# Kernel optimization log

Measured on AMD Instinct MI355X. Metric: run time of the kernel, lower is better.

## Reference

```python
import jax, jax.numpy as jnp
import numpy as np

N = 30000       # mesh nodes
E = 150000      # mesh edges
L = 128         # latent_size
STEPS = 5       # message_passing_steps
TW = 5          # time_window
TD = 2          # target_dim
NODE_IN = TD + 1 + 9   # u + load + node_type one-hot = 12
EDGE_IN = 2 + 1 + TD   # rel_mesh + dist + grad_u = 5


def _mlp(x, W1, b1, W2, b2, g, be):
    # Linear -> ReLU -> Linear -> ReLU -> LayerNorm (matches MLP module)
    h = jax.nn.relu(x @ W1 + b1)
    h = jax.nn.relu(h @ W2 + b2)
    mu = jnp.mean(h, axis=-1, keepdims=True)
    var = jnp.mean(jnp.square(h - mu), axis=-1, keepdims=True)
    return g * (h - mu) / jnp.sqrt(var + 1e-5) + be


def setup_inputs() -> dict:
    key = jax.random.key(0)
    ks = iter(jax.random.split(key, 64))
    def nrm(shape, s=0.05):
        return jax.random.normal(next(ks), shape, dtype=jnp.float32) * s
    inp = {}
    inp['mesh_pos'] = jax.random.normal(next(ks), (1, N, 2), dtype=jnp.float32)
    inp['node_type'] = jax.random.normal(next(ks), (1, N, 9), dtype=jnp.float32)
    inp['u'] = jax.random.normal(next(ks), (1, N, TD), dtype=jnp.float32)
    inp['load'] = jax.random.normal(next(ks), (1, N, 1), dtype=jnp.float32)
    inp['senders'] = jax.random.randint(next(ks), (E,), 0, N, dtype=jnp.int32)
    inp['receivers'] = jax.random.randint(next(ks), (E,), 0, N, dtype=jnp.int32)
    # node encoder MLP(12 -> 128)
    inp['enc_node_W1'] = nrm((NODE_IN, L)); inp['enc_node_b1'] = nrm((L,), 0.01)
    inp['enc_node_W2'] = nrm((L, L));       inp['enc_node_b2'] = nrm((L,), 0.01)
    inp['enc_node_g'] = jnp.ones((L,), jnp.float32); inp['enc_node_be'] = jnp.zeros((L,), jnp.float32)
    # edge encoder MLP(5 -> 128)
    inp['enc_edge_W1'] = nrm((EDGE_IN, L)); inp['enc_edge_b1'] = nrm((L,), 0.01)
    inp['enc_edge_W2'] = nrm((L, L));       inp['enc_edge_b2'] = nrm((L,), 0.01)
    inp['enc_edge_g'] = jnp.ones((L,), jnp.float32); inp['enc_edge_be'] = jnp.zeros((L,), jnp.float32)
    # STEPS GraphNetBlocks, params stacked along leading axis for lax.scan
    inp['blk_edge_W1'] = nrm((STEPS, 3 * L, L)); inp['blk_edge_b1'] = nrm((STEPS, L), 0.01)
    inp['blk_edge_W2'] = nrm((STEPS, L, L));     inp['blk_edge_b2'] = nrm((STEPS, L), 0.01)
    inp['blk_edge_g'] = jnp.ones((STEPS, L), jnp.float32); inp['blk_edge_be'] = jnp.zeros((STEPS, L), jnp.float32)
    inp['blk_node_W1'] = nrm((STEPS, 2 * L, L)); inp['blk_node_b1'] = nrm((STEPS, L), 0.01)
    inp['blk_node_W2'] = nrm((STEPS, L, L));     inp['blk_node_b2'] = nrm((STEPS, L), 0.01)
    inp['blk_node_g'] = jnp.ones((STEPS, L), jnp.float32); inp['blk_node_be'] = jnp.zeros((STEPS, L), jnp.float32)
    # decoder: Conv1d(L,8,1) -> Swish -> Conv1d(8, TD*TW, 1); kernel-size-1 conv == per-node linear
    inp['dec_W1'] = nrm((L, 8)); inp['dec_b1'] = nrm((8,), 0.01)
    inp['dec_W2'] = nrm((8, TD * TW)); inp['dec_b2'] = nrm((TD * TW,), 0.01)
    return inp


def reference(mesh_pos, node_type, u, load, senders, receivers,
              enc_node_W1, enc_node_b1, enc_node_W2, enc_node_b2, enc_node_g, enc_node_be,
              enc_edge_W1, enc_edge_b1, enc_edge_W2, enc_edge_b2, enc_edge_g, enc_edge_be,
              blk_edge_W1, blk_edge_b1, blk_edge_W2, blk_edge_b2, blk_edge_g, blk_edge_be,
              blk_node_W1, blk_node_b1, blk_node_W2, blk_node_b2, blk_node_g, blk_node_be,
              dec_W1, dec_b1, dec_W2, dec_b2):
    # --- encode ---
    node_feats = jnp.concatenate([u, load, node_type], axis=-1)        # [1,N,12]
    nl = _mlp(node_feats, enc_node_W1, enc_node_b1, enc_node_W2, enc_node_b2, enc_node_g, enc_node_be)
    rel = mesh_pos[:, senders] - mesh_pos[:, receivers]                # [1,E,2]
    dist = jnp.linalg.norm(rel, axis=-1, keepdims=True)                # [1,E,1]
    grad_u = u[:, senders] - u[:, receivers]                           # [1,E,2]
    ef = jnp.concatenate([rel, dist, grad_u], axis=-1)                 # [1,E,5]
    el = _mlp(ef, enc_edge_W1, enc_edge_b1, enc_edge_W2, enc_edge_b2, enc_edge_g, enc_edge_be)
    n_nodes = nl.shape[1]

    # --- process: GraphNetBlocks with residual connections ---
    def block(carry, p):
        nl, el = carry
        edge_in = jnp.concatenate([nl[:, senders], nl[:, receivers], el], axis=-1)  # [1,E,3L]
        ne = _mlp(edge_in, p['eW1'], p['eb1'], p['eW2'], p['eb2'], p['eg'], p['ebe'])
        aggr = jax.vmap(lambda e: jax.ops.segment_sum(e, receivers, num_segments=n_nodes))(ne)  # [1,N,L]
        node_in = jnp.concatenate([nl, aggr], axis=-1)                 # [1,N,2L]
        nn = _mlp(node_in, p['nW1'], p['nb1'], p['nW2'], p['nb2'], p['ng'], p['nbe'])
        return (nl + nn, el + ne), None

    ps = {'eW1': blk_edge_W1, 'eb1': blk_edge_b1, 'eW2': blk_edge_W2, 'eb2': blk_edge_b2,
          'eg': blk_edge_g, 'ebe': blk_edge_be,
          'nW1': blk_node_W1, 'nb1': blk_node_b1, 'nW2': blk_node_W2, 'nb2': blk_node_b2,
          'ng': blk_node_g, 'nbe': blk_node_be}
    (nl, el), _ = jax.lax.scan(block, (nl, el), ps)

    # --- decode (1x1 Conv1d == per-node linear) ---
    h = nl @ dec_W1 + dec_b1
    h = h * jax.nn.sigmoid(h)                                          # Swish(beta=1)
    decoded = h @ dec_W2 + dec_b2                                      # [1,N,TW*TD]
    dt = jnp.repeat(jnp.arange(1, TW + 1, dtype=decoded.dtype), TD)    # [TW*TD]
    delta = (decoded * dt).reshape(-1, TW, TD).transpose(1, 0, 2)      # [TW,N,TD]
    return delta
```

## Files before the change

### kernel.cpp

```cpp
#include <hip/hip_runtime.h>
#include <hip/hip_bf16.h>

#define LNUM 128
#define NNODES 30000
#define NEDGES 150000
#define NSTEPS 5


typedef _Float16 f16;
typedef __attribute__((ext_vector_type(2))) _Float16 f16x2;
typedef __attribute__((ext_vector_type(8))) _Float16 f16x8;
typedef __attribute__((ext_vector_type(4))) float f32x4;

__device__ __forceinline__ void glds16(const void* g, void* l) {
    __builtin_amdgcn_global_load_lds(
        (const __attribute__((address_space(1))) void*)g,
        (__attribute__((address_space(3))) void*)l, 16, 0, 0);
}

__device__ __forceinline__ void atomic_pk_add(f16* addr, f16 lo, f16 hi) {
#if __has_builtin(__builtin_amdgcn_global_atomic_fadd_v2f16)
    f16x2 v; v[0] = lo; v[1] = hi;
    __builtin_amdgcn_global_atomic_fadd_v2f16(
        (__attribute__((address_space(1))) f16x2*)addr, v);
#else
    uint32_t* p = (uint32_t*)addr;
    uint32_t old = *p, assumed;
    do {
        assumed = old;
        union { uint32_t u; f16 h[2]; } c; c.u = assumed;
        c.h[0] += lo; c.h[1] += hi;
        old = atomicCAS(p, assumed, c.u);
    } while (old != assumed);
#endif
}

template<int ROWS, int K, int KP>
__device__ __forceinline__ void mlp_apply(
    const float* __restrict__ xs, float* __restrict__ hv,
    float* __restrict__ mu_s, float* __restrict__ rs_s,
    const float* __restrict__ W1, const float* __restrict__ b1,
    const float* __restrict__ W2, const float* __restrict__ b2,
    const float* __restrict__ g,  const float* __restrict__ be,
    float out[ROWS])
{
    const int t = threadIdx.x;
    float acc[ROWS];
    {
        const float bb = b1[t];
        #pragma unroll
        for (int r = 0; r < ROWS; r++) acc[r] = bb;
    }
    int k = 0;
    for (; k + 4 <= K; k += 4) {
        const float w0 = W1[(k + 0) * LNUM + t];
        const float w1 = W1[(k + 1) * LNUM + t];
        const float w2 = W1[(k + 2) * LNUM + t];
        const float w3 = W1[(k + 3) * LNUM + t];
        #pragma unroll
        for (int r = 0; r < ROWS; r++) {
            const float4 x = *(const float4*)(xs + r * KP + k);
            acc[r] = fmaf(x.x, w0, acc[r]);
            acc[r] = fmaf(x.y, w1, acc[r]);
            acc[r] = fmaf(x.z, w2, acc[r]);
            acc[r] = fmaf(x.w, w3, acc[r]);
        }
    }
    for (; k < K; ++k) {
        const float w = W1[k * LNUM + t];
        #pragma unroll
        for (int r = 0; r < ROWS; r++) acc[r] = fmaf(xs[r * KP + k], w, acc[r]);
    }
    #pragma unroll
    for (int r = 0; r < ROWS; r++) hv[r * LNUM + t] = fmaxf(acc[r], 0.f);
    __syncthreads();
    {
        const float bb = b2[t];
        #pragma unroll
        for (int r = 0; r < ROWS; r++) acc[r] = bb;
    }
    for (int k2 = 0; k2 < LNUM; k2 += 4) {
        const float w0 = W2[(k2 + 0) * LNUM + t];
        const float w1 = W2[(k2 + 1) * LNUM + t];
        const float w2 = W2[(k2 + 2) * LNUM + t];
        const float w3 = W2[(k2 + 3) * LNUM + t];
        #pragma unroll
        for (int r = 0; r < ROWS; r++) {
            const float4 x = *(const float4*)(hv + r * LNUM + k2);
            acc[r] = fmaf(x.x, w0, acc[r]);
            acc[r] = fmaf(x.y, w1, acc[r]);
            acc[r] = fmaf(x.z, w2, acc[r]);
            acc[r] = fmaf(x.w, w3, acc[r]);
        }
    }
    __syncthreads();
    #pragma unroll
    for (int r = 0; r < ROWS; r++) hv[r * LNUM + t] = fmaxf(acc[r], 0.f);
    __syncthreads();
    if (t < ROWS) {
        float s = 0.f, s2 = 0.f;
        for (int kk = 0; kk < LNUM; kk++) {
            const float v = hv[t * LNUM + kk];
            s += v; s2 += v * v;
        }
        const float m = s * (1.0f / LNUM);
        mu_s[t] = m;
        rs_s[t] = rsqrtf(fmaxf(s2 * (1.0f / LNUM) - m * m, 0.f) + 1e-5f);
    }
    __syncthreads();
    const float gg = g[t], bbe = be[t];
    #pragma unroll
    for (int r = 0; r < ROWS; r++)
        out[r] = fmaf(gg * (hv[r * LNUM + t] - mu_s[r]), rs_s[r], bbe);
}

__global__ __launch_bounds__(128) void encode_nodes_k(
    const float* __restrict__ u, const float* __restrict__ load_,
    const float* __restrict__ ntype,
    const float* __restrict__ W1, const float* __restrict__ b1,
    const float* __restrict__ W2, const float* __restrict__ b2,
    const float* __restrict__ g,  const float* __restrict__ be,
    f16* __restrict__ nl)
{
    constexpr int ROWS = 4, K = 12, KP = 12;
    __shared__ __align__(16) float xs[ROWS * KP];
    __shared__ __align__(16) float hv[ROWS * LNUM];
    __shared__ float mu_s[ROWS], rs_s[ROWS];
    const int t = threadIdx.x;
    const int base = blockIdx.x * ROWS;
    if (t < ROWS * K) {
        const int r = t / K, k = t % K;
        const int n = base + r;
        float v;
        if (k < 2)      v = u[n * 2 + k];
        else if (k < 3) v = load_[n];
        else            v = ntype[n * 9 + (k - 3)];
        xs[r * KP + k] = v;
    }
    __syncthreads();
    float out[ROWS];
    mlp_apply<ROWS, K, KP>(xs, hv, mu_s, rs_s, W1, b1, W2, b2, g, be, out);
    #pragma unroll
    for (int r = 0; r < ROWS; r++) nl[(base + r) * LNUM + t] = (f16)out[r];
}

#define PE1 245760
#define PE2 81920
#define PN1 163840
#define PN2 81920
#define PQ1 4096
#define PQ2 16384
#define PTOT (PE1+PE2+PN1+PN2+PQ1+PQ2)

__global__ __launch_bounds__(256) void prep_w_all_k(
    const float* __restrict__ eW1, const float* __restrict__ eW2,
    const float* __restrict__ nW1, const float* __restrict__ nW2,
    const float* __restrict__ qW1, const float* __restrict__ qW2,
    f16* __restrict__ out)
{
    int j = blockIdx.x * 256 + threadIdx.x;
    if (j >= PTOT) return;
    const float* W; int K, kreal; f16* hi; f16* p = out;
    if (j < PE1) { W = eW1; K = 384; kreal = 384; hi = p; }
    else { p += PE1; j -= PE1;
    if (j < PE2) { W = eW2; K = 128; kreal = 128; hi = p; }
    else { p += PE2; j -= PE2;
    if (j < PN1) { W = nW1; K = 256; kreal = 256; hi = p; }
    else { p += PN1; j -= PN1;
    if (j < PN2) { W = nW2; K = 128; kreal = 128; hi = p; }
    else { p += PN2; j -= PN2;
    if (j < PQ1) { W = qW1; K = 32;  kreal = 5;   hi = p; }
    else { p += PQ1; j -= PQ1;
         { W = qW2; K = 128; kreal = 128; hi = p; } } } } } }
    const int k = j % K;
    const int rem = j / K;
    const int n = rem & 127;
    const int s = rem >> 7;
    const float v = (k < kreal) ? W[((size_t)s * kreal + k) * 128 + n] : 0.f;
    hi[j] = (f16)v;
}

template<int MODE, int NCH1, int K1S>
__global__ __launch_bounds__(256, 5) void mfma_mlp_k(
    const f16* __restrict__ Lat, const float* __restrict__ Fa,
    const float* __restrict__ Fb,
    f16* __restrict__ io, f16* __restrict__ aggr,
    const int* __restrict__ senders, const int* __restrict__ receivers,
    const f16* __restrict__ W1h, const float* __restrict__ b1,
    const f16* __restrict__ W2h, const float* __restrict__ b2,
    const float* __restrict__ gam, const float* __restrict__ bet,
    int nrows)
{
    __shared__ __align__(16) f16 WH[2][4096];
    __shared__ __align__(16) unsigned short Yh[64 * 128];

    const int t  = threadIdx.x;
    const int w  = t >> 6;
    const int l  = t & 63;
    const int lr = l & 15;
    const int lg = l >> 4;
    const int swz = lg ^ ((lr >> 1) & 3);
    const int base = blockIdx.x * 64;

    const int eg  = base + w * 16 + lr;
    const int egc = min(eg, nrows - 1);

    int sv = 0, rv = 0;
    if constexpr (MODE != 1) { sv = senders[egc]; rv = receivers[egc]; }

    float feat[8];
    if constexpr (MODE == 2) {
        const float ax = Fa[sv * 2], ay = Fa[sv * 2 + 1];
        const float bx = Fa[rv * 2], by = Fa[rv * 2 + 1];
        const float rx = ax - bx, ry = ay - by;
        feat[0] = rx; feat[1] = ry; feat[2] = sqrtf(rx * rx + ry * ry);
        feat[3] = Fb[sv * 2] - Fb[rv * 2];
        feat[4] = Fb[sv * 2 + 1] - Fb[rv * 2 + 1];
        feat[5] = 0.f; feat[6] = 0.f; feat[7] = 0.f;
    }

    auto stage = [&](const f16* __restrict__ Wh, const int kst, const int kc,
                     const int buf) {
        #pragma unroll
        for (int i = 0; i < 2; i++) {
            const int c = 2 * w + i;
            const int ophys = c * 1024 + l * 16;
            const int olog  = ophys ^ (((ophys >> 7) & 3) << 4);
            const int row   = olog >> 6;
            const int slot  = (olog >> 4) & 3;
            glds16(Wh + (size_t)row * kst + kc * 32 + slot * 8,
                   (char*)&WH[buf][0] + c * 1024);
        }
    };

    uint4 qnA, qnB;
    auto prefetchTo = [&](int kc, uint4& q) {
        if constexpr (MODE == 0) {
            const f16* src;
            if (kc < 4)      src = Lat + (size_t)sv  * 128 + kc * 32 + lg * 8;
            else if (kc < 8) src = Lat + (size_t)rv  * 128 + (kc - 4) * 32 + lg * 8;
            else             src = io  + (size_t)egc * 128 + (kc - 8) * 32 + lg * 8;
            q = *(const uint4*)src;
        } else if constexpr (MODE == 1) {
            const f16* src;
            if (kc < 4) src = io  + (size_t)egc * 128 + kc * 32 + lg * 8;
            else        src = Lat + (size_t)egc * 128 + (kc - 4) * 32 + lg * 8;
            q = *(const uint4*)src;
        }
    };

    const f32x4 zero4 = {0.f, 0.f, 0.f, 0.f};
    f32x4 acc[8];
    #pragma unroll
    for (int mf = 0; mf < 8; mf++) acc[mf] = zero4;

    prefetchTo(0, qnA);
    if constexpr (NCH1 > 1) prefetchTo(1, qnB);
    stage(W1h, K1S, 0, 0);
    int cur = 0;

    #pragma unroll
    for (int kc = 0; kc < NCH1; ++kc) {
        __syncthreads();
        if (kc + 1 < NCH1) stage(W1h, K1S, kc + 1, cur ^ 1);
        else               stage(W2h, 128,  0,      cur ^ 1);
        f16x8 XHv, XLv;
        bool useXL = false;
        if constexpr (MODE == 2) {
            union { f16 h[8]; f16x8 v; } uh, ul;
            #pragma unroll
            for (int j = 0; j < 8; j++) {
                const float x = (lg == 0) ? feat[j] : 0.f;
                const f16 h = (f16)x;
                uh.h[j] = h;
                ul.h[j] = (f16)(x - (float)h);
            }
            XHv = uh.v; XLv = ul.v; useXL = true;
        } else {
            union { uint4 q; f16x8 v; } cc;
            cc.q = (kc & 1) ? qnB : qnA;
            XHv = cc.v;
        }
        if (kc + 2 < NCH1) {
            if (kc & 1) prefetchTo(kc + 2, qnB);
            else        prefetchTo(kc + 2, qnA);
        }
        #pragma unroll
        for (int mf = 0; mf < 8; mf++) {
            const int off = (mf * 16 + lr) * 64 + (swz << 4);
            const f16x8 wh = *(const f16x8*)((const char*)&WH[cur][0] + off);
            acc[mf] = __builtin_amdgcn_mfma_f32_16x16x32_f16(XHv, wh, acc[mf], 0, 0, 0);
            if (useXL)
                acc[mf] = __builtin_amdgcn_mfma_f32_16x16x32_f16(XLv, wh, acc[mf], 0, 0, 0);
        }
        cur ^= 1;
    }

    #pragma unroll
    for (int mf = 0; mf < 8; mf++) {
        const float bb1 = b1[mf * 16 + lr];
        #pragma unroll
        for (int reg = 0; reg < 4; reg++) {
            float v = acc[mf][reg] + bb1;
            v = fmaxf(v, 0.f);
            union { f16 h; unsigned short u; } cc; cc.h = (f16)v;
            const int row = w * 16 + lg * 4 + reg;
            const int cb  = (mf * 16 + lr) * 2;
            *(unsigned short*)((char*)Yh + row * 256 +
                               (cb ^ (((lg * 4 + reg) & 7) << 4))) = cc.u;
        }
        acc[mf] = zero4;
    }

    #pragma unroll
    for (int kc = 0; kc < 4; ++kc) {
        __syncthreads();
        if (kc + 1 < 4) stage(W2h, 128, kc + 1, cur ^ 1);
        union { uint4 q; f16x8 v; } YH;
        {
            const int row = w * 16 + lr;
            const int cb  = (kc * 32 + lg * 8) * 2;
            YH.q = *(const uint4*)((const char*)Yh + row * 256 +
                                   (cb ^ ((lr & 7) << 4)));
        }
        #pragma unroll
        for (int mf = 0; mf < 8; mf++) {
            const int off = (mf * 16 + lr) * 64 + (swz << 4);
            const f16x8 wh = *(const f16x8*)((const char*)&WH[cur][0] + off);
            acc[mf] = __builtin_amdgcn_mfma_f32_16x16x32_f16(YH.v, wh, acc[mf], 0, 0, 0);
        }
        cur ^= 1;
    }

    float vv[8][4];
    float s1[4] = {0, 0, 0, 0}, s2[4] = {0, 0, 0, 0};
    #pragma unroll
    for (int mf = 0; mf < 8; mf++) {
        const float bb2 = b2[mf * 16 + lr];
        #pragma unroll
        for (int reg = 0; reg < 4; reg++) {
            float v = acc[mf][reg] + bb2;
            v = fmaxf(v, 0.f);
            vv[mf][reg] = v;
            s1[reg] += v; s2[reg] += v * v;
        }
    }
    #pragma unroll
    for (int m = 1; m < 16; m <<= 1) {
        #pragma unroll
        for (int reg = 0; reg < 4; reg++) {
            s1[reg] += __shfl_xor(s1[reg], m);
            s2[reg] += __shfl_xor(s2[reg], m);
        }
    }
    float gg[8], b8[8];
    #pragma unroll
    for (int mf = 0; mf < 8; mf++) {
        gg[mf] = gam[mf * 16 + lr];
        b8[mf] = bet[mf * 16 + lr];
    }

    #pragma unroll
    for (int reg = 0; reg < 4; reg++) {
        const float mu = s1[reg] * (1.f / 128.f);
        const float rs = rsqrtf(fmaxf(s2[reg] * (1.f / 128.f) - mu * mu, 0.f) + 1e-5f);
        const int row = w * 16 + lg * 4 + reg;
        const int idx = base + row;
        if (idx < nrows) {
            if constexpr (MODE == 0) {
                const int rc = receivers[idx];
                #pragma unroll
                for (int mf = 0; mf < 8; mf++) {
                    const int col = mf * 16 + lr;
                    const float o = gg[mf] * (vv[mf][reg] - mu) * rs + b8[mf];
                    const float op = __shfl_xor(o, 1);
                    if ((lr & 1) == 0)
                        atomic_pk_add(aggr + (size_t)rc * 128 + col,
                                      (f16)o, (f16)op);
                    f16* p = io + (size_t)idx * 128 + col;
                    *p = (f16)((float)*p + o);
                }
            } else if constexpr (MODE == 1) {
                #pragma unroll
                for (int mf = 0; mf < 8; mf++) {
                    const int col = mf * 16 + lr;
                    const float o = gg[mf] * (vv[mf][reg] - mu) * rs + b8[mf];
                    f16* p = io + (size_t)idx * 128 + col;
                    *p = (f16)((float)*p + o);
                }
            } else {
                #pragma unroll
                for (int mf = 0; mf < 8; mf++) {
                    const int col = mf * 16 + lr;
                    const float o = gg[mf] * (vv[mf][reg] - mu) * rs + b8[mf];
                    io[(size_t)idx * 128 + col] = (f16)o;
                }
            }
        }
    }
}

__global__ __launch_bounds__(128) void decode_k(
    const f16* __restrict__ nl,
    const float* __restrict__ W1, const float* __restrict__ b1,
    const float* __restrict__ W2, const float* __restrict__ b2,
    float* __restrict__ out)
{
    constexpr int NPB = 16;
    __shared__ __align__(16) float xs[NPB * LNUM];
    __shared__ float hh[NPB * 8];
    const int t = threadIdx.x;
    const int base = blockIdx.x * NPB;
    for (int r = 0; r < NPB; r++) xs[r * LNUM + t] = (float)nl[(base + r) * LNUM + t];
    __syncthreads();
    {
        const int node = t >> 3, j = t & 7;
        float a = b1[j];
        for (int k = 0; k < LNUM; k++) a = fmaf(xs[node * LNUM + k], W1[k * 8 + j], a);
        hh[node * 8 + j] = a / (1.f + expf(-a));
    }
    __syncthreads();
    for (int idx = t; idx < NPB * 10; idx += 128) {
        const int node = idx / 10, c = idx % 10;
        float a = b2[c];
        #pragma unroll
        for (int j = 0; j < 8; j++) a = fmaf(hh[node * 8 + j], W2[j * 10 + c], a);
        const int tt = c >> 1, d = c & 1;
        out[(size_t)tt * (NNODES * 2) + (size_t)(base + node) * 2 + d] =
            a * (float)(tt + 1);
    }
}

__global__ __launch_bounds__(256) void zero_k(float* __restrict__ p, int n)
{
    const int i = blockIdx.x * 256 + threadIdx.x;
    if (i < n) p[i] = 0.f;
}

extern "C" void kernel_launch(void* const* d_in, const int* in_sizes, int n_in,
                              void* d_out, int out_size, void* d_ws, size_t ws_size,
                              hipStream_t stream) {
    const float* F[34];
    for (int i = 0; i < 34; i++) F[i] = (const float*)d_in[i];
    const int* senders   = (const int*)d_in[4];
    const int* receivers = (const int*)d_in[5];

    const size_t nN = (size_t)NNODES * LNUM;
    const size_t nE = (size_t)NEDGES * LNUM;
    f16* nl16   = (f16*)d_ws;
    f16* el16   = nl16 + nN;
    f16* aggr16 = el16 + nE;
    f16* wb     = aggr16 + nN;
    f16 *eW1h = wb;
    f16 *eW2h = eW1h + PE1;
    f16 *nW1h = eW2h + PE2;
    f16 *nW2h = nW1h + PN1;
    f16 *qW1h = nW2h + PN2;
    f16 *qW2h = qW1h + PQ1;

    prep_w_all_k<<<(PTOT + 255) / 256, 256, 0, stream>>>(
        F[18], F[20], F[24], F[26], F[12], F[14], wb);

    encode_nodes_k<<<NNODES / 4, 128, 0, stream>>>(
        F[2], F[3], F[1], F[6], F[7], F[8], F[9], F[10], F[11], nl16);

    const int egrid = (NEDGES + 63) / 64;
    const int ngrid = (NNODES + 63) / 64;

    mfma_mlp_k<2, 1, 32><<<egrid, 256, 0, stream>>>(
        nullptr, F[0], F[2], el16, nullptr, senders, receivers,
        qW1h, F[13], qW2h, F[15], F[16], F[17], NEDGES);

    for (int s = 0; s < NSTEPS; s++) {
        zero_k<<<(NNODES * 64 + 255) / 256, 256, 0, stream>>>(
            (float*)aggr16, NNODES * 64);
        mfma_mlp_k<0, 12, 384><<<egrid, 256, 0, stream>>>(
            nl16, nullptr, nullptr, el16, aggr16, senders, receivers,
            eW1h + (size_t)s * 384 * 128, F[19] + s * LNUM,
            eW2h + (size_t)s * 128 * 128, F[21] + s * LNUM,
            F[22] + s * LNUM, F[23] + s * LNUM, NEDGES);
        mfma_mlp_k<1, 8, 256><<<ngrid, 256, 0, stream>>>(
            aggr16, nullptr, nullptr, nl16, nullptr, nullptr, nullptr,
            nW1h + (size_t)s * 256 * 128, F[25] + s * LNUM,
            nW2h + (size_t)s * 128 * 128, F[27] + s * LNUM,
            F[28] + s * LNUM, F[29] + s * LNUM, NNODES);
    }

    decode_k<<<NNODES / 16, 128, 0, stream>>>(
        nl16, F[30], F[31], F[32], F[33], (float*)d_out);
}
```

Baseline: 830.0 us.

## Use triple-buffered activation prefetch with partial vmcnt waits and fuse aggr zeroing

Replaces __syncthreads in the K loops with explicit s_waitcnt vmcnt(1)/vmcnt(0) plus raw s_barrier, so one activation prefetch can stay in flight across the barrier. The activation prefetch moves to a three-register rotation issued earlier in each iteration. The per-step zero_k launch is removed: the node MLP kernel now clears its aggr rows after reading them, and only one initial zeroing remains. This saves kernel launches and an extra pass over memory, but relies on hand-counted vmcnt ordering that could race if the compiler reorders loads.

```diff
diff --git a/kernel.cpp b/kernel.cpp
--- a/kernel.cpp
+++ b/kernel.cpp
@@ -233,7 +233,7 @@
         }
     };
 
-    uint4 qnA, qnB;
+    uint4 qnA, qnB, qnC;
     auto prefetchTo = [&](int kc, uint4& q) {
         if constexpr (MODE == 0) {
             const f16* src;
@@ -254,16 +254,30 @@
     #pragma unroll
     for (int mf = 0; mf < 8; mf++) acc[mf] = zero4;
 
-    prefetchTo(0, qnA);
-    if constexpr (NCH1 > 1) prefetchTo(1, qnB);
+    if constexpr (MODE != 2) {
+        prefetchTo(0, qnA);
+        if constexpr (NCH1 > 1) prefetchTo(1, qnB);
+    }
     stage(W1h, K1S, 0, 0);
-    int cur = 0;
 
     #pragma unroll
     for (int kc = 0; kc < NCH1; ++kc) {
-        __syncthreads();
-        if (kc + 1 < NCH1) stage(W1h, K1S, kc + 1, cur ^ 1);
-        else               stage(W2h, 128,  0,      cur ^ 1);
+        if (MODE != 2 && kc >= 1 && kc + 1 < NCH1)
+            asm volatile("s_waitcnt vmcnt(1)" ::: "memory");
+        else
+            asm volatile("s_waitcnt vmcnt(0)" ::: "memory");
+        __builtin_amdgcn_sched_barrier(0);
+        __builtin_amdgcn_s_barrier();
+        __builtin_amdgcn_sched_barrier(0);
+        if (kc + 1 < NCH1) stage(W1h, K1S, kc + 1, (kc + 1) & 1);
+        else               stage(W2h, 128,  0,      NCH1 & 1);
+        if constexpr (MODE != 2) {
+            if (kc + 2 < NCH1) {
+                if      ((kc + 2) % 3 == 0) prefetchTo(kc + 2, qnA);
+                else if ((kc + 2) % 3 == 1) prefetchTo(kc + 2, qnB);
+                else                        prefetchTo(kc + 2, qnC);
+            }
+        }
         f16x8 XHv, XLv;
         bool useXL = false;
         if constexpr (MODE == 2) {
@@ -278,22 +292,17 @@
             XHv = uh.v; XLv = ul.v; useXL = true;
         } else {
             union { uint4 q; f16x8 v; } cc;
-            cc.q = (kc & 1) ? qnB : qnA;
+            cc.q = (kc % 3 == 0) ? qnA : ((kc % 3 == 1) ? qnB : qnC);
             XHv = cc.v;
-        }
-        if (kc + 2 < NCH1) {
-            if (kc & 1) prefetchTo(kc + 2, qnB);
-            else        prefetchTo(kc + 2, qnA);
         }
         #pragma unroll
         for (int mf = 0; mf < 8; mf++) {
             const int off = (mf * 16 + lr) * 64 + (swz << 4);
-            const f16x8 wh = *(const f16x8*)((const char*)&WH[cur][0] + off);
+            const f16x8 wh = *(const f16x8*)((const char*)&WH[kc & 1][0] + off);
             acc[mf] = __builtin_amdgcn_mfma_f32_16x16x32_f16(XHv, wh, acc[mf], 0, 0, 0);
             if (useXL)
                 acc[mf] = __builtin_amdgcn_mfma_f32_16x16x32_f16(XLv, wh, acc[mf], 0, 0, 0);
         }
-        cur ^= 1;
     }
 
     #pragma unroll
@@ -314,8 +323,11 @@
 
     #pragma unroll
     for (int kc = 0; kc < 4; ++kc) {
-        __syncthreads();
-        if (kc + 1 < 4) stage(W2h, 128, kc + 1, cur ^ 1);
+        asm volatile("s_waitcnt vmcnt(0)" ::: "memory");
+        __builtin_amdgcn_sched_barrier(0);
+        __builtin_amdgcn_s_barrier();
+        __builtin_amdgcn_sched_barrier(0);
+        if (kc + 1 < 4) stage(W2h, 128, kc + 1, (NCH1 + kc + 1) & 1);
         union { uint4 q; f16x8 v; } YH;
         {
             const int row = w * 16 + lr;
@@ -326,10 +338,9 @@
         #pragma unroll
         for (int mf = 0; mf < 8; mf++) {
             const int off = (mf * 16 + lr) * 64 + (swz << 4);
-            const f16x8 wh = *(const f16x8*)((const char*)&WH[cur][0] + off);
+            const f16x8 wh = *(const f16x8*)((const char*)&WH[(NCH1 + kc) & 1][0] + off);
             acc[mf] = __builtin_amdgcn_mfma_f32_16x16x32_f16(YH.v, wh, acc[mf], 0, 0, 0);
         }
-        cur ^= 1;
     }
 
     float vv[8][4];
@@ -398,6 +409,13 @@
             }
         }
     }
+
+    if constexpr (MODE == 1) {
+        const uint4 z = {0, 0, 0, 0};
+        #pragma unroll
+        for (int c = 0; c < 4; c++)
+            *(uint4*)(aggr + (size_t)egc * 128 + c * 32 + lg * 8) = z;
+    }
 }
 
 __global__ __launch_bounds__(128) void decode_k(
@@ -471,16 +489,17 @@
         nullptr, F[0], F[2], el16, nullptr, senders, receivers,
         qW1h, F[13], qW2h, F[15], F[16], F[17], NEDGES);
 
+    zero_k<<<(NNODES * 64 + 255) / 256, 256, 0, stream>>>(
+        (float*)aggr16, NNODES * 64);
+
     for (int s = 0; s < NSTEPS; s++) {
-        zero_k<<<(NNODES * 64 + 255) / 256, 256, 0, stream>>>(
-            (float*)aggr16, NNODES * 64);
         mfma_mlp_k<0, 12, 384><<<egrid, 256, 0, stream>>>(
             nl16, nullptr, nullptr, el16, aggr16, senders, receivers,
             eW1h + (size_t)s * 384 * 128, F[19] + s * LNUM,
             eW2h + (size_t)s * 128 * 128, F[21] + s * LNUM,
             F[22] + s * LNUM, F[23] + s * LNUM, NEDGES);
         mfma_mlp_k<1, 8, 256><<<ngrid, 256, 0, stream>>>(
-            aggr16, nullptr, nullptr, nl16, nullptr, nullptr, nullptr,
+            aggr16, nullptr, nullptr, nl16, aggr16, nullptr, nullptr,
             nW1h + (size_t)s * 256 * 128, F[25] + s * LNUM,
             nW2h + (size_t)s * 128 * 128, F[27] + s * LNUM,
             F[28] + s * LNUM, F[29] + s * LNUM, NNODES);
```

Result: faster. 807.6 us (-2.7%).
